# Kernel tuning notes

Hardware: AMD Instinct MI355X
Metric: run time of the kernel (lower is better)

Reference implementation:

```python
import jax, jax.numpy as jnp
import numpy as np

B, T, I, H, K = 32, 1024, 512, 512, 2


def _causal_conv1d(x_bit, w_hik, b_h):
    # x_bit: [B, I, T]; left-pad K-1 zeros (ConstantPad1d((K-1, 0)))
    xp = jnp.pad(x_bit, ((0, 0), (0, 0), (K - 1, 0)))
    y = jax.lax.conv_general_dilated(
        xp, w_hik, window_strides=(1,), padding='VALID',
        dimension_numbers=('NCH', 'OIH', 'NCH'))  # [B, H, T]
    return y + b_h[None, :, None]


def setup_inputs() -> dict:
    key = jax.random.key(0)
    k1, k2, k3 = jax.random.split(key, 3)
    bound = 1.0 / np.sqrt(I * K)  # torch Conv1d default init scale
    return {
        'inputs': jax.random.normal(k1, (B, T, I), dtype=jnp.float32),
        'init_state': jnp.zeros((B, H), dtype=jnp.float32),
        'Wz': jax.random.uniform(k2, (H, I, K), jnp.float32, -bound, bound),
        'bz': jnp.zeros((H,), dtype=jnp.float32),
        'Wf': jax.random.uniform(k3, (H, I, K), jnp.float32, -bound, bound),
        'bf': jnp.zeros((H,), dtype=jnp.float32),
    }


def reference(inputs, init_state, Wz, bz, Wf, bf):
    # init_state is accepted but unused in the original forward (mode='f').
    x = inputs.transpose(0, 2, 1)                      # [B, I, T]
    raw_f = _causal_conv1d(x, Wf, bf).transpose(0, 2, 1)  # [B, T, H]
    raw_z = _causal_conv1d(x, Wz, bz).transpose(0, 2, 1)  # [B, T, H]

    log_f = jax.nn.log_sigmoid(raw_f)
    log_one_minus_f = jax.nn.log_sigmoid(-raw_f)
    log_z = jax.nn.log_sigmoid(raw_z)

    # recurrent_gates[t] = sum_{s>t} log_f[s]  (suffix sum of log_f over time, excluding t=0 shift)
    rg = log_f[:, 1:, :]                               # [B, T-1, H]
    cs = jnp.cumsum(rg, axis=1)
    rg = rg - cs + cs[:, -1:, :]
    rg = jnp.concatenate([rg, jnp.zeros((inputs.shape[0], 1, rg.shape[2]), dtype=rg.dtype)], axis=1)  # [B, T, H]

    log_hidden = jax.lax.cumlogsumexp(log_z + log_one_minus_f + rg, axis=1)
    hidden = jnp.exp(log_hidden - rg)
    return hidden
```

## Files before the change

### kernel.cpp

```cpp
#include <hip/hip_runtime.h>
#include <hip/hip_bf16.h>
#include <cstddef>
#include <cstdint>

#define B_  32
#define T_  1024
#define I_  512
#define H_  512
#define M_  (B_ * T_)
#define TP_ 1025

typedef __bf16 bf16x8  __attribute__((ext_vector_type(8)));
typedef float  floatx4 __attribute__((ext_vector_type(4)));
typedef unsigned short ushort8v __attribute__((ext_vector_type(8)));
typedef unsigned long long u64;

__device__ __forceinline__ unsigned short f2bf(float f) {
    uint32_t u = __float_as_uint(f);
    return (unsigned short)((u + 0x7FFFu + ((u >> 16) & 1u)) >> 16);
}
__device__ __forceinline__ float sigm(float x) {
    return __builtin_amdgcn_rcpf(1.f + __expf(-x));
}

#define GLL(src, dst) __builtin_amdgcn_global_load_lds( \
    (const __attribute__((address_space(1))) void*)(src), \
    (__attribute__((address_space(3))) void*)(dst), 16, 0, 0)

#define NB_BUILD 8200
#define NB_PACK  512
#define NB_ZERO  256

__global__ __launch_bounds__(256) void prep(const float* __restrict__ x,
                                            const float* __restrict__ Wf,
                                            const float* __restrict__ Wz,
                                            unsigned short* __restrict__ Ab2,
                                            unsigned short* __restrict__ Wq,
                                            uint4* __restrict__ HpubZ,
                                            uint32_t* __restrict__ cnt) {
    if (blockIdx.x < NB_BUILD) {
        int g = blockIdx.x * 256 + threadIdx.x;
        int idx8 = g << 3;
        int row = idx8 >> 9;
        int col = idx8 & 511;
        int b    = (int)((unsigned)row / TP_);
        int trow = row - b * TP_;
        ushort8v o = {0, 0, 0, 0, 0, 0, 0, 0};
        if (trow > 0) {
            const float* src = &x[((size_t)b * T_ + (trow - 1)) * I_ + col];
            float4 v0 = *(const float4*)src;
            float4 v1 = *(const float4*)(src + 4);
            o[0] = f2bf(v0.x); o[1] = f2bf(v0.y); o[2] = f2bf(v0.z); o[3] = f2bf(v0.w);
            o[4] = f2bf(v1.x); o[5] = f2bf(v1.y); o[6] = f2bf(v1.z); o[7] = f2bf(v1.w);
        }
        *(ushort8v*)&Ab2[(size_t)idx8] = o;
    } else if (blockIdx.x < NB_BUILD + NB_PACK) {
        int cid = (blockIdx.x - NB_BUILD) * 256 + threadIdx.x;
        int lane = cid & 63;
        int c    = (cid >> 6) & 3;
        int wn   = (cid >> 8) & 1;
        int ksub = (cid >> 9) & 31;
        int ni   = (cid >> 14) & 3;
        int gate = (cid >> 16) & 1;
        int n_col = ni * 128 + wn * 64 + c * 16 + (lane & 15);
        const float* G = gate ? Wz : Wf;
        ushort8v o;
        #pragma unroll
        for (int j = 0; j < 8; ++j) {
            int k   = ksub * 32 + (lane >> 4) * 8 + j;
            int tap = k >> 9;
            int i   = k & 511;
            o[j] = f2bf(G[n_col * (I_ * 2) + i * 2 + tap]);
        }
        *(ushort8v*)&Wq[(size_t)cid * 8] = o;
    } else {
        int g = (blockIdx.x - NB_BUILD - NB_PACK) * 256 + threadIdx.x;
        HpubZ[g] = make_uint4(0, 0, 0, 0);
        if (g == 0) *cnt = 0;
    }
}

__global__ __launch_bounds__(256, 2) void mfma_gemm_scan(
        const unsigned short* __restrict__ Ab2,
        const unsigned short* __restrict__ Wq,
        const float* __restrict__ biasF,
        const float* __restrict__ biasZ,
        float* __restrict__ out,
        u64* __restrict__ Hpub,
        uint32_t* __restrict__ counter) {
    __shared__ unsigned short smem[24576];
    __shared__ uint32_t vid_s;

    const int tid = threadIdx.x;
    if (tid == 0) vid_s = atomicAdd(counter, 1u);
    __syncthreads();
    const int vid   = (int)vid_s;
    const int low3  = vid & 7;
    const int ni    = (vid >> 3) & 3;
    const int rem   = vid >> 5;
    const int pos   = rem >> 2;
    const int b     = ((rem & 3) << 3) | low3;
    const int chain = ni * 32 + b;
    const int h0    = ni * 128;
    const int browBase = b * TP_ + pos * 128;

    const int lane = tid & 63;
    const int wave = tid >> 6;
    const int wm   = wave >> 1, wn = wave & 1;
    const int lm   = lane & 15, quad = lane >> 4;

    const int c0 = wave * 128 + lane;
    const int c1 = c0 + 64;
    const int r0 = c0 >> 2, q0 = (c0 & 3) ^ ((r0 >> 2) & 3);
    const int r1 = c1 >> 2, q1 = (c1 & 3) ^ ((r1 >> 2) & 3);

    const unsigned short* pA0 = Ab2 + (size_t)(browBase + r0) * 512 + q0 * 8;
    const unsigned short* pA1 = Ab2 + (size_t)(browBase + r1) * 512 + q1 * 8;

    unsigned short* dA0 = smem + wave * 1024;
    unsigned short* dA1 = smem + wave * 1024 + 512;

    const unsigned short* wq = Wq + ni * 131072 + wn * 2048 + lane * 8;

    int offA[4];
    #pragma unroll
    for (int r = 0; r < 4; ++r) {
        int ml = wm * 64 + r * 16 + lm;
        offA[r] = (4 * ml + (quad ^ ((ml >> 2) & 3))) * 8;
    }

    floatx4 accF[4][4] = {};
    floatx4 accZ[4][4] = {};

    for (int kt2 = 0; kt2 < 16; ++kt2) {
        const int tap = kt2 >> 3;
        const int i0  = (kt2 & 7) * 64;
        #pragma unroll
        for (int s = 0; s < 2; ++s) {
            const int aoff = tap * 512 + i0 + s * 32;
            GLL(pA0 + aoff, dA0 + s * 4096);
            GLL(pA1 + aoff, dA1 + s * 4096);
        }
        __syncthreads();

        #pragma unroll
        for (int s = 0; s < 2; ++s) {
            const int ksub = kt2 * 2 + s;
            const unsigned short* wqk = wq + ksub * 4096;
            bf16x8 af[4], bF[4], bZ[4];
            #pragma unroll
            for (int c = 0; c < 4; ++c) {
                bF[c] = *(const bf16x8*)(wqk + c * 512);
                bZ[c] = *(const bf16x8*)(wqk + 524288 + c * 512);
            }
            #pragma unroll
            for (int r = 0; r < 4; ++r) af[r] = *(const bf16x8*)(smem + s * 4096 + offA[r]);
            #pragma unroll
            for (int r = 0; r < 4; ++r) {
                #pragma unroll
                for (int c = 0; c < 4; ++c) {
                    accF[r][c] = __builtin_amdgcn_mfma_f32_16x16x32_bf16(
                                    af[r], bF[c], accF[r][c], 0, 0, 0);
                    accZ[r][c] = __builtin_amdgcn_mfma_f32_16x16x32_bf16(
                                    af[r], bZ[c], accZ[r][c], 0, 0, 0);
                }
            }
        }
        __syncthreads();
    }

    float bfv[4], bzv[4];
    #pragma unroll
    for (int c = 0; c < 4; ++c) {
        int hc = h0 + wn * 64 + c * 16 + lm;
        bfv[c] = biasF[hc];
        bzv[c] = biasZ[hc];
    }

    float2* seg  = (float2*)smem;
    float*  hinL = (float*)&smem[16384];

    #pragma unroll
    for (int r = 0; r < 4; ++r) {
        const int sid = wm * 16 + r * 4 + quad;
        #pragma unroll
        for (int c = 0; c < 4; ++c) {
            float A = 1.f, C = 0.f;
            #pragma unroll
            for (int v = 0; v < 4; ++v) {
                float f = sigm(accF[r][c][v] + bfv[c]);
                float z = sigm(accZ[r][c][v] + bzv[c]);
                accF[r][c][v] = f;
                accZ[r][c][v] = z;
                A *= f;
                C = fmaf(f, C - z, z);
            }
            seg[sid * 128 + wn * 64 + c * 16 + lm] = make_float2(A, C);
        }
    }
    __syncthreads();

    float Hin = 0.f;
    if (tid < 128) {
        float At = 1.f, Ct = 0.f;
        #pragma unroll 8
        for (int s = 0; s < 32; ++s) {
            float2 sc = seg[s * 128 + tid];
            Ct = fmaf(sc.x, Ct, sc.y);
            At *= sc.x;
        }
        if (pos > 0) {
            u64* p = &Hpub[((size_t)(pos - 1) * 128 + chain) * 128 + tid];
            u64 v;
            while (((v = atomicAdd(p, 0ull)) >> 32) == 0ull)
                __builtin_amdgcn_s_sleep(2);
            Hin = __uint_as_float((uint32_t)v);
        }
        if (pos < 7) {
            float Hout = fmaf(At, Hin, Ct);
            u64 pv = 0x100000000ull | (u64)__float_as_uint(Hout);
            atomicExch(&Hpub[((size_t)pos * 128 + chain) * 128 + tid], pv);
        }
        float run = Hin;
        #pragma unroll 8
        for (int s = 0; s < 32; ++s) {
            hinL[s * 128 + tid] = run;
            float2 sc = seg[s * 128 + tid];
            run = fmaf(sc.x, run, sc.y);
        }
    }
    __syncthreads();

    const int rowBase = b * T_ + pos * 128;
    #pragma unroll
    for (int r = 0; r < 4; ++r) {
        const int sid = wm * 16 + r * 4 + quad;
        #pragma unroll
        for (int c = 0; c < 4; ++c) {
            const int hc = h0 + wn * 64 + c * 16 + lm;
            float hs = hinL[sid * 128 + (hc - h0)];
            #pragma unroll
            for (int v = 0; v < 4; ++v) {
                float f = accF[r][c][v];
                float z = accZ[r][c][v];
                hs = fmaf(f, hs - z, z);
                const size_t row = (size_t)(rowBase + wm * 64 + r * 16 + quad * 4 + v);
                out[row * H_ + hc] = hs;
            }
        }
    }
}

extern "C" void kernel_launch(void* const* d_in, const int* in_sizes, int n_in,
                              void* d_out, int out_size, void* d_ws, size_t ws_size,
                              hipStream_t stream) {
    const float* x  = (const float*)d_in[0];
    const float* Wz = (const float*)d_in[2];
    const float* bz = (const float*)d_in[3];
    const float* Wf = (const float*)d_in[4];
    const float* bf = (const float*)d_in[5];
    float* out = (float*)d_out;

    char* ws = (char*)d_ws;
    unsigned short* Ab2  = (unsigned short*)(ws);
    unsigned short* Wq   = (unsigned short*)(ws + (size_t)34 * 1024 * 1024);
    u64*            Hpub = (u64*)(ws + (size_t)36 * 1024 * 1024);
    uint32_t*       cnt  = (uint32_t*)(ws + (size_t)37 * 1024 * 1024);

    prep<<<NB_BUILD + NB_PACK + NB_ZERO, 256, 0, stream>>>(
        x, Wf, Wz, Ab2, Wq, (uint4*)Hpub, cnt);

    mfma_gemm_scan<<<1024, 256, 0, stream>>>(Ab2, Wq, bf, bz, out, Hpub, cnt);
}
```

Before: 201.6 us.

## Triple-buffer A tiles in LDS with async prefetch two stages ahead

Replaces the synchronous load-then-compute loop with a three-buffer LDS ring. Global-to-LDS loads for tile k+2 are issued during the MFMA work on tile k, and explicit vmcnt waits replace the double __syncthreads per iteration. It also raises wave priority around the MFMA blocks. This should hide global-load latency behind the matrix math. In exchange it uses more LDS, which could lower occupancy, and relies on hand-tuned waitcnt counts whose correctness depends on the exact load count per stage.

```diff
diff --git a/kernel.cpp b/kernel.cpp
--- a/kernel.cpp
+++ b/kernel.cpp
@@ -117,9 +117,6 @@
     const unsigned short* pA0 = Ab2 + (size_t)(browBase + r0) * 512 + q0 * 8;
     const unsigned short* pA1 = Ab2 + (size_t)(browBase + r1) * 512 + q1 * 8;
 
-    unsigned short* dA0 = smem + wave * 1024;
-    unsigned short* dA1 = smem + wave * 1024 + 512;
-
     const unsigned short* wq = Wq + ni * 131072 + wn * 2048 + lane * 8;
 
     int offA[4];
@@ -132,42 +129,81 @@
     floatx4 accF[4][4] = {};
     floatx4 accZ[4][4] = {};
 
+#define ISSUE(t, dst) do {                                              \
+        const int aoff_ = (((t) >> 3) * 512) + (((t) & 7) * 64);        \
+        unsigned short* d_ = (dst) + wave * 1024;                       \
+        GLL(pA0 + aoff_,      d_);                                      \
+        GLL(pA1 + aoff_,      d_ + 512);                                \
+        GLL(pA0 + aoff_ + 32, d_ + 4096);                               \
+        GLL(pA1 + aoff_ + 32, d_ + 4608);                               \
+    } while (0)
+
+    ISSUE(0, smem);
+    ISSUE(1, smem + 8192);
+
+    unsigned short* b0 = smem;
+    unsigned short* b1 = smem + 8192;
+    unsigned short* b2 = smem + 16384;
+
     for (int kt2 = 0; kt2 < 16; ++kt2) {
-        const int tap = kt2 >> 3;
-        const int i0  = (kt2 & 7) * 64;
-        #pragma unroll
-        for (int s = 0; s < 2; ++s) {
-            const int aoff = tap * 512 + i0 + s * 32;
-            GLL(pA0 + aoff, dA0 + s * 4096);
-            GLL(pA1 + aoff, dA1 + s * 4096);
-        }
-        __syncthreads();
-
-        #pragma unroll
-        for (int s = 0; s < 2; ++s) {
-            const int ksub = kt2 * 2 + s;
-            const unsigned short* wqk = wq + ksub * 4096;
-            bf16x8 af[4], bF[4], bZ[4];
+        if (kt2 < 15) asm volatile("s_waitcnt vmcnt(4)");
+        else          asm volatile("s_waitcnt vmcnt(0)");
+        __builtin_amdgcn_s_barrier();
+        asm volatile("" ::: "memory");
+
+        const unsigned short* wqk0 = wq + (kt2 * 2) * 4096;
+        bf16x8 af0[4], bF0[4], bZ0[4];
+        #pragma unroll
+        for (int r = 0; r < 4; ++r) af0[r] = *(const bf16x8*)(b0 + offA[r]);
+        #pragma unroll
+        for (int c = 0; c < 4; ++c) {
+            bF0[c] = *(const bf16x8*)(wqk0 + c * 512);
+            bZ0[c] = *(const bf16x8*)(wqk0 + 524288 + c * 512);
+        }
+        __builtin_amdgcn_s_setprio(1);
+        #pragma unroll
+        for (int r = 0; r < 4; ++r) {
             #pragma unroll
             for (int c = 0; c < 4; ++c) {
-                bF[c] = *(const bf16x8*)(wqk + c * 512);
-                bZ[c] = *(const bf16x8*)(wqk + 524288 + c * 512);
+                accF[r][c] = __builtin_amdgcn_mfma_f32_16x16x32_bf16(
+                                af0[r], bF0[c], accF[r][c], 0, 0, 0);
+                accZ[r][c] = __builtin_amdgcn_mfma_f32_16x16x32_bf16(
+                                af0[r], bZ0[c], accZ[r][c], 0, 0, 0);
             }
+        }
+        __builtin_amdgcn_s_setprio(0);
+
+        const unsigned short* wqk1 = wqk0 + 4096;
+        bf16x8 af1[4], bF1[4], bZ1[4];
+        #pragma unroll
+        for (int r = 0; r < 4; ++r) af1[r] = *(const bf16x8*)(b0 + 4096 + offA[r]);
+        #pragma unroll
+        for (int c = 0; c < 4; ++c) {
+            bF1[c] = *(const bf16x8*)(wqk1 + c * 512);
+            bZ1[c] = *(const bf16x8*)(wqk1 + 524288 + c * 512);
+        }
+        if (kt2 < 14) {
+            __builtin_amdgcn_sched_barrier(0);
+            ISSUE(kt2 + 2, b2);
+            __builtin_amdgcn_sched_barrier(0);
+        }
+        __builtin_amdgcn_s_setprio(1);
+        #pragma unroll
+        for (int r = 0; r < 4; ++r) {
             #pragma unroll
-            for (int r = 0; r < 4; ++r) af[r] = *(const bf16x8*)(smem + s * 4096 + offA[r]);
-            #pragma unroll
-            for (int r = 0; r < 4; ++r) {
-                #pragma unroll
-                for (int c = 0; c < 4; ++c) {
-                    accF[r][c] = __builtin_amdgcn_mfma_f32_16x16x32_bf16(
-                                    af[r], bF[c], accF[r][c], 0, 0, 0);
-                    accZ[r][c] = __builtin_amdgcn_mfma_f32_16x16x32_bf16(
-                                    af[r], bZ[c], accZ[r][c], 0, 0, 0);
-                }
+            for (int c = 0; c < 4; ++c) {
+                accF[r][c] = __builtin_amdgcn_mfma_f32_16x16x32_bf16(
+                                af1[r], bF1[c], accF[r][c], 0, 0, 0);
+                accZ[r][c] = __builtin_amdgcn_mfma_f32_16x16x32_bf16(
+                                af1[r], bZ1[c], accZ[r][c], 0, 0, 0);
             }
         }
-        __syncthreads();
-    }
+        __builtin_amdgcn_s_setprio(0);
+
+        unsigned short* t_ = b0; b0 = b1; b1 = b2; b2 = t_;
+    }
+#undef ISSUE
+    __syncthreads();
 
     float bfv[4], bzv[4];
     #pragma unroll
```

Result: no change. 200.0 us (-0.8%).

## Triple-buffer A and B tiles in LDS with async loads and MFMA priority

Applied to the files above, without the earlier changes.

The GEMM main loop becomes a three-stage software pipeline. Both the activation tile and the weight tile now stream into LDS through asynchronous global-to-LDS loads, two k-steps ahead, with one barrier per step and vmcnt waits instead of two __syncthreads per iteration. Weights used to be read straight from global memory into registers, and the MFMA block now runs at raised wave priority via s_setprio. The goal is to hide global load latency behind MFMA work, at the cost of more LDS per block (which may reduce how many blocks fit per CU) and fragile hand-written vmcnt accounting.

```diff
diff --git a/kernel.cpp b/kernel.cpp
--- a/kernel.cpp
+++ b/kernel.cpp
@@ -88,7 +88,7 @@
         float* __restrict__ out,
         u64* __restrict__ Hpub,
         uint32_t* __restrict__ counter) {
-    __shared__ unsigned short smem[24576];
+    __shared__ unsigned short smem[36864];
     __shared__ uint32_t vid_s;
 
     const int tid = threadIdx.x;
@@ -117,10 +117,8 @@
     const unsigned short* pA0 = Ab2 + (size_t)(browBase + r0) * 512 + q0 * 8;
     const unsigned short* pA1 = Ab2 + (size_t)(browBase + r1) * 512 + q1 * 8;
 
-    unsigned short* dA0 = smem + wave * 1024;
-    unsigned short* dA1 = smem + wave * 1024 + 512;
-
-    const unsigned short* wq = Wq + ni * 131072 + wn * 2048 + lane * 8;
+    const unsigned short* pB = Wq + (size_t)(wave >> 1) * 524288
+                                  + ni * 131072 + (wave & 1) * 2048 + lane * 8;
 
     int offA[4];
     #pragma unroll
@@ -128,46 +126,75 @@
         int ml = wm * 64 + r * 16 + lm;
         offA[r] = (4 * ml + (quad ^ ((ml >> 2) & 3))) * 8;
     }
+    const int offBF = wn * 4 * 512 + lane * 8;
+    const int offBZ = (8 + wn * 4) * 512 + lane * 8;
 
     floatx4 accF[4][4] = {};
     floatx4 accZ[4][4] = {};
 
-    for (int kt2 = 0; kt2 < 16; ++kt2) {
-        const int tap = kt2 >> 3;
-        const int i0  = (kt2 & 7) * 64;
-        #pragma unroll
-        for (int s = 0; s < 2; ++s) {
-            const int aoff = tap * 512 + i0 + s * 32;
-            GLL(pA0 + aoff, dA0 + s * 4096);
-            GLL(pA1 + aoff, dA1 + s * 4096);
-        }
-        __syncthreads();
-
-        #pragma unroll
-        for (int s = 0; s < 2; ++s) {
-            const int ksub = kt2 * 2 + s;
-            const unsigned short* wqk = wq + ksub * 4096;
-            bf16x8 af[4], bF[4], bZ[4];
-            #pragma unroll
-            for (int c = 0; c < 4; ++c) {
-                bF[c] = *(const bf16x8*)(wqk + c * 512);
-                bZ[c] = *(const bf16x8*)(wqk + 524288 + c * 512);
-            }
-            #pragma unroll
-            for (int r = 0; r < 4; ++r) af[r] = *(const bf16x8*)(smem + s * 4096 + offA[r]);
-            #pragma unroll
-            for (int r = 0; r < 4; ++r) {
-                #pragma unroll
-                for (int c = 0; c < 4; ++c) {
-                    accF[r][c] = __builtin_amdgcn_mfma_f32_16x16x32_bf16(
-                                    af[r], bF[c], accF[r][c], 0, 0, 0);
-                    accZ[r][c] = __builtin_amdgcn_mfma_f32_16x16x32_bf16(
-                                    af[r], bZ[c], accZ[r][c], 0, 0, 0);
-                }
-            }
-        }
-        __syncthreads();
-    }
+#define ISSUE(ksub, sA, sB) do {                                        \
+        const int aoff_ = (((ksub) >> 4) * 512) + (((ksub) & 15) * 32); \
+        GLL(pA0 + aoff_, (sA) + wave * 1024);                           \
+        GLL(pA1 + aoff_, (sA) + wave * 1024 + 512);                     \
+        const unsigned short* bs_ = pB + (ksub) * 4096;                 \
+        unsigned short* bd_ = (sB) + wave * 4 * 512;                    \
+        GLL(bs_,        bd_);                                           \
+        GLL(bs_ + 512,  bd_ + 512);                                     \
+        GLL(bs_ + 1024, bd_ + 1024);                                    \
+        GLL(bs_ + 1536, bd_ + 1536);                                    \
+    } while (0)
+
+#define COMPUTE(sA, sB) do {                                            \
+        bf16x8 af_[4], bF_[4], bZ_[4];                                  \
+        _Pragma("unroll")                                               \
+        for (int c = 0; c < 4; ++c) {                                   \
+            bF_[c] = *(const bf16x8*)((sB) + offBF + c * 512);          \
+            bZ_[c] = *(const bf16x8*)((sB) + offBZ + c * 512);          \
+        }                                                               \
+        _Pragma("unroll")                                               \
+        for (int r = 0; r < 4; ++r)                                     \
+            af_[r] = *(const bf16x8*)((sA) + offA[r]);                  \
+        __builtin_amdgcn_s_setprio(1);                                  \
+        _Pragma("unroll")                                               \
+        for (int r = 0; r < 4; ++r) {                                   \
+            _Pragma("unroll")                                           \
+            for (int c = 0; c < 4; ++c) {                               \
+                accF[r][c] = __builtin_amdgcn_mfma_f32_16x16x32_bf16(   \
+                                af_[r], bF_[c], accF[r][c], 0, 0, 0);   \
+                accZ[r][c] = __builtin_amdgcn_mfma_f32_16x16x32_bf16(   \
+                                af_[r], bZ_[c], accZ[r][c], 0, 0, 0);   \
+            }                                                           \
+        }                                                               \
+        __builtin_amdgcn_s_setprio(0);                                  \
+    } while (0)
+
+    unsigned short* s0 = smem;
+    unsigned short* s1 = smem + 12288;
+    unsigned short* s2 = smem + 24576;
+
+    ISSUE(0, s0, s0 + 4096);
+    ISSUE(1, s1, s1 + 4096);
+
+    for (int k = 0; k < 30; ++k) {
+        asm volatile("s_waitcnt vmcnt(6)");
+        __builtin_amdgcn_s_barrier();
+        asm volatile("" ::: "memory");
+        ISSUE(k + 2, s2, s2 + 4096);
+        COMPUTE(s0, s0 + 4096);
+        unsigned short* t_ = s0; s0 = s1; s1 = s2; s2 = t_;
+    }
+    asm volatile("s_waitcnt vmcnt(6)");
+    __builtin_amdgcn_s_barrier();
+    asm volatile("" ::: "memory");
+    COMPUTE(s0, s0 + 4096);
+    { unsigned short* t_ = s0; s0 = s1; s1 = s2; s2 = t_; }
+    asm volatile("s_waitcnt vmcnt(0)");
+    __builtin_amdgcn_s_barrier();
+    asm volatile("" ::: "memory");
+    COMPUTE(s0, s0 + 4096);
+#undef ISSUE
+#undef COMPUTE
+    __syncthreads();
 
     float bfv[4], bzv[4];
     #pragma unroll
@@ -257,8 +284,8 @@
     const float* x  = (const float*)d_in[0];
     const float* Wz = (const float*)d_in[2];
     const float* bz = (const float*)d_in[3];
+    const float* bf = (const float*)d_in[5];
     const float* Wf = (const float*)d_in[4];
-    const float* bf = (const float*)d_in[5];
     float* out = (float*)d_out;
 
     char* ws = (char*)d_ws;
```

New measurement: 203.5 us. No clear change (+0.9%).
